# Optimization experiments

Hardware: AMD Instinct MI355X
Metric: run time of the kernel (lower is better)

## Reference

```python
import jax, jax.numpy as jnp
import numpy as np

B, T, K, H, KS = 8, 2048, 64, 8, 5
PAD = KS - 1  # causal left padding (kernel_size - stride, stride=1)


def setup_inputs() -> dict:
    key = jax.random.key(0)
    ks = jax.random.split(key, 6)
    s = 0.02
    return {
        "x": jax.random.normal(ks[0], (B, T, K), jnp.float32),
        "wq": jax.random.normal(ks[1], (K * H, K, KS), jnp.float32) * s,
        "bq": jnp.zeros((K * H,), jnp.float32),
        "wk": jax.random.normal(ks[2], (K * H, K, KS), jnp.float32) * s,
        "bk": jnp.zeros((K * H,), jnp.float32),
        "wv": jax.random.normal(ks[3], (K * H, K, KS), jnp.float32) * s,
        "wu": jax.random.normal(ks[4], (K, K * H), jnp.float32) * s,
        "bu": jnp.zeros((K,), jnp.float32),
    }


def _causal_conv(x_bkt, w, b=None):
    # x_bkt: [b, k, t]; w: [out_ch, in_ch, ks]; left-pad for causality
    y = jax.lax.conv_general_dilated(
        x_bkt, w, window_strides=(1,), padding=[(PAD, 0)],
        dimension_numbers=("NCH", "OIH", "NCH"))
    if b is not None:
        y = y + b[None, :, None]
    return y


def reference(x, wq, bq, wk, bk, wv, wu, bu):
    b, t, k = x.shape
    xc = jnp.transpose(x, (0, 2, 1))  # [b, k, t]
    # conv output channels k*h are viewed as (k, h): head index varies fastest
    q = _causal_conv(xc, wq, bq).reshape(b, k, H, t)
    kk = _causal_conv(xc, wk, bk).reshape(b, k, H, t)
    v = _causal_conv(xc, wv).reshape(b, k, H, t)
    scale = k ** 0.25
    # scores: [b, h, t_q, t_k]
    w = jnp.einsum("bdht,bdhs->bhts", q / scale, kk / scale)
    mask = jnp.triu(jnp.ones((t, t), bool), 1)  # mask_next=True, mask_diag=False
    w = jnp.where(mask[None, None], -jnp.inf, w)
    w = jax.nn.softmax(w, axis=-1)
    out = jnp.einsum("bhts,bdhs->bthd", w, v)  # [b, t, h, k]
    out = out.reshape(b, t, H * k)  # concat order (h outer, k inner)
    return out @ wu.T + bu
```

## Files before the change

kernel.cpp:

```cpp
#include <hip/hip_runtime.h>
#include <hip/hip_bf16.h>

typedef __attribute__((ext_vector_type(8))) short bf16x8;
typedef __attribute__((ext_vector_type(4))) float f32x4;
typedef __attribute__((ext_vector_type(16))) float f32x16;
typedef __attribute__((ext_vector_type(4))) unsigned int u32x4;
typedef __attribute__((ext_vector_type(2))) unsigned int u32x2;

#define Bn 8
#define Tn 2048
#define Kn 64
#define Hn 8
#define KSn 5
#define CHn 512
#define TPADn 2052

__device__ __forceinline__ unsigned short f2bf(float f) {
    unsigned int x = __builtin_bit_cast(unsigned int, f);
    unsigned int r = (x + 0x7fffu + ((x >> 16) & 1u)) >> 16;
    return (unsigned short)r;
}

__device__ __forceinline__ unsigned int cvt_pk_bf16(float lo, float hi) {
    unsigned int r;
    asm("v_cvt_pk_bf16_f32 %0, %1, %2" : "=v"(r) : "v"(lo), "v"(hi));
    return r;
}

__device__ __forceinline__ float fast_exp2(float x) {
#if __has_builtin(__builtin_amdgcn_exp2f)
    return __builtin_amdgcn_exp2f(x);
#else
    float r;
    asm("v_exp_f32 %0, %1" : "=v"(r) : "v"(x));
    return r;
#endif
}

__device__ __forceinline__ float xhalf_max(float v) {
    return fmaxf(v, __shfl_xor(v, 32));
}
__device__ __forceinline__ float xhalf_add(float v) {
    return v + __shfl_xor(v, 32);
}

__device__ __forceinline__ u32x2 pl32swap(unsigned int x, unsigned int y) {
#if __has_builtin(__builtin_amdgcn_permlane32_swap)
    return __builtin_amdgcn_permlane32_swap(x, y, false, false);
#else
    unsigned int xs = (unsigned int)__shfl_xor((int)x, 32);
    unsigned int ys = (unsigned int)__shfl_xor((int)y, 32);
    int hi = (threadIdx.x & 63) >> 5;
    u32x2 r;
    r[0] = hi ? ys : x;
    r[1] = hi ? y : xs;
    return r;
#endif
}

__device__ __forceinline__ void gload_lds16(const void* g, void* l) {
    __builtin_amdgcn_global_load_lds(
        (const __attribute__((address_space(1))) void*)g,
        (__attribute__((address_space(3))) void*)l, 16, 0, 0);
}

__global__ void prep_kernel(const float* __restrict__ x,
                            const float* __restrict__ wq, const float* __restrict__ bq,
                            const float* __restrict__ wk, const float* __restrict__ bk,
                            const float* __restrict__ wv,
                            const float* __restrict__ wu,
                            unsigned short* __restrict__ x_pad,
                            unsigned short* __restrict__ w2q, unsigned short* __restrict__ w2k,
                            unsigned short* __restrict__ w2v,
                            unsigned short* __restrict__ wu_b,
                            float* __restrict__ bqs, float* __restrict__ bks)
{
    const float inv_scale = 0.424660900144f;
    const int N0 = Bn*TPADn*Kn;
    const int N1 = KSn*CHn*Kn;
    const int total = N0 + 3*N1 + CHn*Kn + 2*CHn;
    for (int i = blockIdx.x*blockDim.x + threadIdx.x; i < total; i += gridDim.x*blockDim.x) {
        if (i < N0) {
            int b = i / (TPADn*Kn);
            int rem = i - b*(TPADn*Kn);
            int p = rem >> 6, ic = rem & 63;
            x_pad[i] = (p < 4) ? (unsigned short)0
                               : f2bf(x[((size_t)b*Tn + (p - 4))*Kn + ic]);
            continue;
        }
        int r = i - N0;
        if (r < 3*N1) {
            int conv = r / N1; int rr = r - conv*N1;
            int j = rr / (CHn*Kn); int rc = rr - j*(CHn*Kn);
            int c = rc >> 6; int ic = rc & 63;
            const float* w = (conv==0) ? wq : ((conv==1) ? wk : wv);
            float s = (conv==2) ? 1.0f : inv_scale;
            unsigned short* dst = (conv==0) ? w2q : ((conv==1) ? w2k : w2v);
            dst[rr] = f2bf(w[(c*Kn + ic)*KSn + j] * s);
            continue;
        }
        r -= 3*N1;
        if (r < CHn*Kn) { wu_b[r] = f2bf(wu[r]); continue; }
        r -= CHn*Kn;
        if (r < CHn) { bqs[r] = bq[r]*inv_scale; continue; }
        r -= CHn;
        bks[r] = bk[r]*inv_scale;
    }
}

__global__ __launch_bounds__(256) void conv_v4(
    const unsigned short* __restrict__ x_pad,
    const unsigned short* __restrict__ w2q, const unsigned short* __restrict__ w2k,
    const unsigned short* __restrict__ w2v,
    const float* __restrict__ bqs, const float* __restrict__ bks,
    unsigned short* __restrict__ q_s, unsigned short* __restrict__ k_s,
    unsigned short* __restrict__ v_t)
{
    __shared__ __align__(16) unsigned short xs[2][72*64];
    __shared__ __align__(16) unsigned short ts[64*64];
    const int tg = blockIdx.x;
    const int c0 = blockIdx.y * 64;
    const int zz = blockIdx.z;
    const int conv = zz >> 3, b = zz & 7;
    const unsigned short* w2 = (conv==0) ? w2q : ((conv==1) ? w2k : w2v);
    const float* bias = (conv==0) ? bqs : ((conv==1) ? bks : nullptr);
    unsigned short* outp = (conv==0) ? q_s : ((conv==1) ? k_s : v_t);
    const int tid = threadIdx.x;
    const int wid = tid >> 6, l = tid & 63;
    const int lr = l & 15, lh = l >> 4;
    const int wt = wid & 1, wc = wid >> 1;

    bf16x8 wf[5][2][2];
    #pragma unroll
    for (int j = 0; j < 5; ++j)
        #pragma unroll
        for (int kk = 0; kk < 2; ++kk)
            #pragma unroll
            for (int n2 = 0; n2 < 2; ++n2)
                wf[j][kk][n2] = *(const bf16x8*)
                    &w2[(j*CHn + c0 + wc*32 + n2*16 + lr)*Kn + kk*32 + lh*8];
    float bv0 = bias ? bias[c0 + wc*32 + lr]      : 0.0f;
    float bv1 = bias ? bias[c0 + wc*32 + 16 + lr] : 0.0f;

    const int swz_row = l >> 3;
    const int src_inrow = ((l & 7) << 4) ^ (swz_row << 4);

    int buf = 0;
    {
        const char* base = (const char*)(x_pad + (size_t)b*TPADn*Kn);
        int p0 = tg*512;
        for (int i = wid; i < 9; i += 4) {
            const char* src = base + (size_t)(p0 + i*8 + swz_row)*128 + src_inrow;
            gload_lds16(src, (char*)&xs[0][0] + i*1024);
        }
    }
    __syncthreads();

    for (int tt = 0; tt < 8; ++tt) {
        const int t0 = (tg*8 + tt)*64;
        if (tt < 7) {
            const char* base = (const char*)(x_pad + (size_t)b*TPADn*Kn);
            int p0 = t0 + 64;
            for (int i = wid; i < 9; i += 4) {
                const char* src = base + (size_t)(p0 + i*8 + swz_row)*128 + src_inrow;
                gload_lds16(src, (char*)&xs[buf^1][0] + i*1024);
            }
        }
        const char* xb = (const char*)&xs[buf][0];
        f32x4 acc[2][2] = {};
        #pragma unroll
        for (int j = 0; j < 5; ++j)
            #pragma unroll
            for (int kk = 0; kk < 2; ++kk) {
                #pragma unroll
                for (int m = 0; m < 2; ++m) {
                    int row = wt*32 + m*16 + lr + j;
                    bf16x8 a = *(const bf16x8*)
                        (xb + row*128 + ((kk*64 + lh*16) ^ ((row & 7) << 4)));
                    acc[m][0] = __builtin_amdgcn_mfma_f32_16x16x32_bf16(a, wf[j][kk][0], acc[m][0], 0, 0, 0);
                    acc[m][1] = __builtin_amdgcn_mfma_f32_16x16x32_bf16(a, wf[j][kk][1], acc[m][1], 0, 0, 0);
                }
            }
        __syncthreads();
        #pragma unroll
        for (int m = 0; m < 2; ++m)
            #pragma unroll
            for (int n2 = 0; n2 < 2; ++n2) {
                float bv = n2 ? bv1 : bv0;
                int cl = wc*32 + n2*16 + lr;
                #pragma unroll
                for (int reg = 0; reg < 4; ++reg) {
                    int tl = wt*32 + m*16 + lh*4 + reg;
                    ts[(tl*64 + cl) ^ ((tl & 7) << 3)] = f2bf(acc[m][n2][reg] + bv);
                }
            }
        __syncthreads();
        if (conv < 2) {
            #pragma unroll
            for (int it = 0; it < 2; ++it) {
                int idx = tid + it*256;
                int tl = idx >> 3, hl = idx & 7;
                unsigned short tmp[8];
                #pragma unroll
                for (int dl = 0; dl < 8; ++dl)
                    tmp[dl] = ts[(tl*64 + hl + 8*dl) ^ ((tl & 7) << 3)];
                size_t el = ((size_t)(b*Hn + hl)*Tn + t0 + tl)*Kn + (c0 >> 3);
                *(u32x4*)&outp[el] = *(u32x4*)tmp;
            }
        } else {
            #pragma unroll
            for (int it = 0; it < 2; ++it) {
                int idx = tid + it*256;
                int tc = idx >> 6, cl2 = idx & 63;
                int hl = cl2 & 7, dl = cl2 >> 3;
                unsigned short tmp[8];
                #pragma unroll
                for (int i2 = 0; i2 < 8; ++i2)
                    tmp[i2] = ts[((tc*8 + i2)*64 + cl2) ^ (((tc*8 + i2) & 7) << 3)];
                size_t el = ((size_t)(b*Hn + hl)*Kn + (c0 >> 3) + dl)*Tn + t0 + tc*8;
                *(u32x4*)&outp[el] = *(u32x4*)tmp;
            }
        }
        buf ^= 1;
    }
}

__global__ __launch_bounds__(256, 3) void attn_kernel(
    const unsigned short* __restrict__ q_s, const unsigned short* __restrict__ k_s,
    const unsigned short* __restrict__ v_t, unsigned short* __restrict__ attn2)
{
    __shared__ __align__(16) unsigned char lds_raw[32768];
    const int tid = threadIdx.x;
    const int wid = tid >> 6, l = tid & 63;
    const int lq = l & 31, hi = l >> 5;
    const int bx = blockIdx.x;
    const int bh = (bx & 7)*8 + ((bx >> 3) & 7);
    const int kb = bx >> 6;
    int c, t0, t1, role;
    if (kb < 24) {
        c = (wid < 2) ? (16 + kb) : (63 - kb);
        int L = c + 1, mid = L >> 1, h = wid & 1;
        t0 = h ? mid : 0; t1 = h ? L : mid;
        role = h ? 2 : 1;
    } else {
        int i = kb - 24;
        c = (wid == 0) ? i : (wid == 1) ? 7 - i : (wid == 2) ? 8 + i : 15 - i;
        t0 = 0; t1 = c + 1; role = 0;
    }
    const int qw = c * 32;
    const unsigned short* qp = q_s + (size_t)bh*Tn*Kn;
    const char* kpc = (const char*)(k_s + (size_t)bh*Tn*Kn);
    const char* vpc = (const char*)(v_t + (size_t)bh*Kn*Tn);
    unsigned short* op = attn2 + (size_t)bh*Tn*Kn;
    const int qg = qw + lq;

    char* stK = (char*)lds_raw + wid*8192;
    char* stV = stK + 4096;

    const int kSrcOff = (l >> 3)*128 + (((l & 7) ^ (l >> 3)) << 4);
    const int vSrcOff = (l >> 3)*8192 + ((l >> 2) & 1)*4096
                      + ((((l & 3) ^ ((l >> 3) & 3))) << 4);
    const char* ktp = kpc + (size_t)t0*4096 + kSrcOff;
    const char* vtp = vpc + (size_t)t0*64   + vSrcOff;
    auto stage = [&]() {
        gload_lds16(ktp,           stK);
        gload_lds16(ktp + 1024,    stK + 1024);
        gload_lds16(ktp + 2048,    stK + 2048);
        gload_lds16(ktp + 3072,    stK + 3072);
        gload_lds16(vtp,           stV);
        gload_lds16(vtp + 65536,   stV + 1024);
        gload_lds16(vtp + 131072,  stV + 2048);
        gload_lds16(vtp + 196608,  stV + 3072);
        ktp += 4096; vtp += 64;
    };

    bf16x8 qf[4];
    #pragma unroll
    for (int m = 0; m < 4; ++m)
        qf[m] = *(const bf16x8*)&qp[(qw + lq)*Kn + m*16 + hi*8];

    f32x16 o0 = (f32x16)(0.0f), o1 = (f32x16)(0.0f);
    float m_run = -1e30f, l_run = 0.f;

    const int vReadBase = (lq >> 1)*128 + (lq & 1)*64;
    const int vSwz = (lq >> 1) & 3;

    stage();
    for (int t = t0; t < t1; ++t) {
        asm volatile("s_waitcnt vmcnt(0)" ::: "memory");
        __builtin_amdgcn_sched_barrier(0);
        bf16x8 kbf[4], vbf[2][2];
        #pragma unroll
        for (int m = 0; m < 4; ++m)
            kbf[m] = *(const bf16x8*)(stK + lq*128 + ((m*32 + hi*16) ^ ((lq & 7) << 4)));
        #pragma unroll
        for (int dn = 0; dn < 2; ++dn)
            #pragma unroll
            for (int ks = 0; ks < 2; ++ks)
                vbf[dn][ks] = *(const bf16x8*)
                    (stV + dn*2048 + vReadBase + (((ks*2 + hi) ^ vSwz) << 4));
        asm volatile("s_waitcnt lgkmcnt(0)" ::: "memory");
        __builtin_amdgcn_sched_barrier(0);
        if (t + 1 < t1) stage();
        __builtin_amdgcn_sched_barrier(0);
        const int s0 = t*32;
        f32x16 s = (f32x16)(0.0f);
        #pragma unroll
        for (int m = 0; m < 4; ++m)
            s = __builtin_amdgcn_mfma_f32_32x32x16_bf16(kbf[m], qf[m], s, 0, 0, 0);
        if (t == c) {
            #pragma unroll
            for (int r = 0; r < 16; ++r) {
                int sg = s0 + (r & 3) + 8*(r >> 2) + 4*hi;
                if (sg > qg) s[r] = -1e30f;
            }
        }
        float a8[8];
        #pragma unroll
        for (int r = 0; r < 8; ++r) a8[r] = fmaxf(s[r], s[r + 8]);
        float a4_0 = fmaxf(a8[0], a8[4]), a4_1 = fmaxf(a8[1], a8[5]);
        float a4_2 = fmaxf(a8[2], a8[6]), a4_3 = fmaxf(a8[3], a8[7]);
        float mt = fmaxf(fmaxf(a4_0, a4_1), fmaxf(a4_2, a4_3));
        mt = xhalf_max(mt);
        if (!__all(mt <= m_run + 8.0f)) {
            float mn = fmaxf(m_run, mt);
            float alpha = fast_exp2(m_run - mn);
            m_run = mn;
            l_run *= alpha;
            #pragma unroll
            for (int r = 0; r < 16; ++r) { o0[r] *= alpha; o1[r] *= alpha; }
        }
        float ps[4] = {0.f, 0.f, 0.f, 0.f};
        #pragma unroll
        for (int r = 0; r < 16; ++r) {
            float p = fast_exp2(s[r] - m_run);
            s[r] = p;
            ps[r & 3] += p;
        }
        l_run += (ps[0] + ps[1]) + (ps[2] + ps[3]);
        unsigned int W[8];
        #pragma unroll
        for (int rp = 0; rp < 8; ++rp)
            W[rp] = cvt_pk_bf16(s[2*rp], s[2*rp + 1]);
        u32x4 bw[2];
        #pragma unroll
        for (int m = 0; m < 2; ++m)
            #pragma unroll
            for (int jp = 0; jp < 2; ++jp) {
                u32x2 sw = pl32swap(W[jp + 4*m], W[jp + 4*m + 2]);
                bw[m][jp]     = sw[0];
                bw[m][jp + 2] = sw[1];
            }
        o0 = __builtin_amdgcn_mfma_f32_32x32x16_bf16(vbf[0][0], __builtin_bit_cast(bf16x8, bw[0]), o0, 0, 0, 0);
        o0 = __builtin_amdgcn_mfma_f32_32x32x16_bf16(vbf[0][1], __builtin_bit_cast(bf16x8, bw[1]), o0, 0, 0, 0);
        o1 = __builtin_amdgcn_mfma_f32_32x32x16_bf16(vbf[1][0], __builtin_bit_cast(bf16x8, bw[0]), o1, 0, 0, 0);
        o1 = __builtin_amdgcn_mfma_f32_32x32x16_bf16(vbf[1][1], __builtin_bit_cast(bf16x8, bw[1]), o1, 0, 0, 0);
    }

    if (role == 2) {
        float* po = (float*)stK;
        #pragma unroll
        for (int r = 0; r < 16; ++r) {
            po[r*64 + l]        = o0[r];
            po[(16 + r)*64 + l] = o1[r];
        }
    }
    if (role) __syncthreads();
    if (role == 2) {
        float* pml = (float*)(lds_raw + (wid - 1)*8192);
        pml[l] = m_run; pml[64 + l] = l_run;
    }
    if (role) __syncthreads();
    if (role == 2) return;
    if (role == 1) {
        const float* po  = (const float*)(lds_raw + (wid + 1)*8192);
        const float* pml = (const float*)(lds_raw + wid*8192);
        float m2 = pml[l], l2 = pml[64 + l];
        float mf = fmaxf(m_run, m2);
        float a1 = fast_exp2(m_run - mf), a2 = fast_exp2(m2 - mf);
        l_run = l_run*a1 + l2*a2;
        #pragma unroll
        for (int r = 0; r < 16; ++r) {
            o0[r] = o0[r]*a1 + po[r*64 + l]*a2;
            o1[r] = o1[r]*a1 + po[(16 + r)*64 + l]*a2;
        }
    }

    float l_full = xhalf_add(l_run);
    char* myLds = stK;
    float inv_l = 1.0f / l_full;
    #pragma unroll
    for (int e = 0; e < 16; e += 2) {
        int dd = (e & 3) + 8*(e >> 2) + 4*hi;
        unsigned int wv0 = cvt_pk_bf16(o0[e]*inv_l, o0[e+1]*inv_l);
        *(unsigned int*)(myLds + ((lq*128 + dd*2)      ^ ((lq & 7) << 4))) = wv0;
        unsigned int wv1 = cvt_pk_bf16(o1[e]*inv_l, o1[e+1]*inv_l);
        *(unsigned int*)(myLds + ((lq*128 + 64 + dd*2) ^ ((lq & 7) << 4))) = wv1;
    }
    int q2 = l >> 1, hf = l & 1;
    #pragma unroll
    for (int o4 = 0; o4 < 4; ++o4) {
        u32x4 vr2 = *(u32x4*)(myLds + ((q2*128 + hf*64 + o4*16) ^ ((q2 & 7) << 4)));
        *(u32x4*)&op[(qw + q2)*Kn + hf*32 + o4*8] = vr2;
    }
}

__global__ __launch_bounds__(256) void proj_kernel(
    const unsigned short* __restrict__ attn, const unsigned short* __restrict__ wu_b,
    const float* __restrict__ bu, float* __restrict__ outp)
{
    __shared__ float red[4*16*66];
    const int r0 = blockIdx.x * 16;
    const int tid = threadIdx.x;
    const int w = tid >> 6, l = tid & 63;
    const int lr = l & 15, lh = l >> 4;
    f32x4 acc[4] = {};
    const int r = r0 + lr;
    const int bb = r >> 11, tt = r & 2047;
    #pragma unroll
    for (int ki = 0; ki < 4; ++ki) {
        int kk = w*4 + ki;
        int ch = kk*32 + lh*8;
        int hh = ch >> 6, dd = ch & 63;
        bf16x8 a = *(const bf16x8*)&attn[(size_t)((bb*Hn + hh)*Tn + tt)*Kn + dd];
        #pragma unroll
        for (int n = 0; n < 4; ++n) {
            bf16x8 bf = *(const bf16x8*)&wu_b[(n*16 + lr)*CHn + ch];
            acc[n] = __builtin_amdgcn_mfma_f32_16x16x32_bf16(a, bf, acc[n], 0, 0, 0);
        }
    }
    #pragma unroll
    for (int n = 0; n < 4; ++n)
        #pragma unroll
        for (int reg = 0; reg < 4; ++reg)
            red[w*1056 + (lh*4 + reg)*66 + n*16 + lr] = acc[n][reg];
    __syncthreads();
    #pragma unroll
    for (int it = 0; it < 4; ++it) {
        int idx = tid + it*256;
        int rl = idx >> 6, ko = idx & 63;
        float s = red[rl*66 + ko] + red[1056 + rl*66 + ko]
                + red[2112 + rl*66 + ko] + red[3168 + rl*66 + ko] + bu[ko];
        outp[(size_t)(r0 + rl)*Kn + ko] = s;
    }
}

extern "C" void kernel_launch(void* const* d_in, const int* in_sizes, int n_in,
                              void* d_out, int out_size, void* d_ws, size_t ws_size,
                              hipStream_t stream)
{
    const float* x  = (const float*)d_in[0];
    const float* wq = (const float*)d_in[1];
    const float* bq = (const float*)d_in[2];
    const float* wk = (const float*)d_in[3];
    const float* bk = (const float*)d_in[4];
    const float* wv = (const float*)d_in[5];
    const float* wu = (const float*)d_in[6];
    const float* bu = (const float*)d_in[7];
    float* outp = (float*)d_out;

    char* ws = (char*)d_ws;
    size_t off = 0;
    auto alloc = [&](size_t bytes) {
        char* p = ws + off;
        off = (off + bytes + 255) & ~(size_t)255;
        return p;
    };
    unsigned short* x_pad = (unsigned short*)alloc((size_t)Bn*TPADn*Kn*2);
    unsigned short* w2q  = (unsigned short*)alloc((size_t)KSn*CHn*Kn*2);
    unsigned short* w2k  = (unsigned short*)alloc((size_t)KSn*CHn*Kn*2);
    unsigned short* w2v  = (unsigned short*)alloc((size_t)KSn*CHn*Kn*2);
    unsigned short* wu_b = (unsigned short*)alloc((size_t)CHn*Kn*2);
    float*  bqs = (float*)alloc(CHn*4);
    float*  bks = (float*)alloc(CHn*4);
    unsigned short* q_s  = (unsigned short*)alloc((size_t)Bn*Hn*Tn*Kn*2);
    unsigned short* k_s  = (unsigned short*)alloc((size_t)Bn*Hn*Tn*Kn*2);
    unsigned short* v_t  = (unsigned short*)alloc((size_t)Bn*Hn*Tn*Kn*2);
    unsigned short* attn = (unsigned short*)alloc((size_t)Bn*Tn*CHn*2);

    prep_kernel<<<2048, 256, 0, stream>>>(x, wq, bq, wk, bk, wv, wu,
                                          x_pad, w2q, w2k, w2v, wu_b, bqs, bks);
    conv_v4<<<dim3(4, 8, 24), 256, 0, stream>>>(
        x_pad, w2q, w2k, w2v, bqs, bks, q_s, k_s, v_t);
    attn_kernel<<<1792, 256, 0, stream>>>(q_s, k_s, v_t, attn);
    proj_kernel<<<(Bn*Tn)/16, 256, 0, stream>>>(attn, wu_b, bu, outp);
}
```

Before: 126.9 us.

## Process two key tiles per attention iteration with doubled LDS staging

The attention inner loop now stages and handles two 32-wide key/value tiles per iteration. It runs both score MFMAs, then a single combined max/rescale step and the PV MFMAs for both tiles, with a single-tile tail for odd counts. This halves the per-tile waits, barriers and online-softmax rescale overhead and gives more independent MFMA work between memory waits. In exchange, LDS use doubles to 64KB and launch bounds drop from 3 to 2 blocks per CU, which lowers occupancy and adds register pressure.

```diff
diff --git a/kernel.cpp b/kernel.cpp
--- a/kernel.cpp
+++ b/kernel.cpp
@@ -225,11 +225,11 @@
     }
 }
 
-__global__ __launch_bounds__(256, 3) void attn_kernel(
+__global__ __launch_bounds__(256, 2) void attn_kernel(
     const unsigned short* __restrict__ q_s, const unsigned short* __restrict__ k_s,
     const unsigned short* __restrict__ v_t, unsigned short* __restrict__ attn2)
 {
-    __shared__ __align__(16) unsigned char lds_raw[32768];
+    __shared__ __align__(16) unsigned char lds_raw[65536];
     const int tid = threadIdx.x;
     const int wid = tid >> 6, l = tid & 63;
     const int lq = l & 31, hi = l >> 5;
@@ -254,8 +254,9 @@
     unsigned short* op = attn2 + (size_t)bh*Tn*Kn;
     const int qg = qw + lq;
 
-    char* stK = (char*)lds_raw + wid*8192;
-    char* stV = stK + 4096;
+    char* slot = (char*)lds_raw + wid*16384;
+    char* stK = slot;
+    char* stV = slot + 8192;
 
     const int kSrcOff = (l >> 3)*128 + (((l & 7) ^ (l >> 3)) << 4);
     const int vSrcOff = (l >> 3)*8192 + ((l >> 2) & 1)*4096
@@ -267,11 +268,19 @@
         gload_lds16(ktp + 1024,    stK + 1024);
         gload_lds16(ktp + 2048,    stK + 2048);
         gload_lds16(ktp + 3072,    stK + 3072);
+        gload_lds16(ktp + 4096,    stK + 4096);
+        gload_lds16(ktp + 5120,    stK + 5120);
+        gload_lds16(ktp + 6144,    stK + 6144);
+        gload_lds16(ktp + 7168,    stK + 7168);
         gload_lds16(vtp,           stV);
         gload_lds16(vtp + 65536,   stV + 1024);
         gload_lds16(vtp + 131072,  stV + 2048);
         gload_lds16(vtp + 196608,  stV + 3072);
-        ktp += 4096; vtp += 64;
+        gload_lds16(vtp + 64,           stV + 4096);
+        gload_lds16(vtp + 64 + 65536,   stV + 5120);
+        gload_lds16(vtp + 64 + 131072,  stV + 6144);
+        gload_lds16(vtp + 64 + 196608,  stV + 7168);
+        ktp += 8192; vtp += 128;
     };
 
     bf16x8 qf[4];
@@ -282,17 +291,110 @@
     f32x16 o0 = (f32x16)(0.0f), o1 = (f32x16)(0.0f);
     float m_run = -1e30f, l_run = 0.f;
 
+    const int kReadBase = lq*128;
+    const int kReadSwz  = (lq & 7) << 4;
     const int vReadBase = (lq >> 1)*128 + (lq & 1)*64;
     const int vSwz = (lq >> 1) & 3;
 
     stage();
-    for (int t = t0; t < t1; ++t) {
+    int t = t0;
+    while (t + 1 < t1) {
+        asm volatile("s_waitcnt vmcnt(0)" ::: "memory");
+        __builtin_amdgcn_sched_barrier(0);
+        bf16x8 k0[4], k1[4], v0[2][2], v1[2][2];
+        #pragma unroll
+        for (int m = 0; m < 4; ++m) {
+            k0[m] = *(const bf16x8*)(stK +        kReadBase + ((m*32 + hi*16) ^ kReadSwz));
+            k1[m] = *(const bf16x8*)(stK + 4096 + kReadBase + ((m*32 + hi*16) ^ kReadSwz));
+        }
+        #pragma unroll
+        for (int dn = 0; dn < 2; ++dn)
+            #pragma unroll
+            for (int ks = 0; ks < 2; ++ks) {
+                v0[dn][ks] = *(const bf16x8*)
+                    (stV +        dn*2048 + vReadBase + (((ks*2 + hi) ^ vSwz) << 4));
+                v1[dn][ks] = *(const bf16x8*)
+                    (stV + 4096 + dn*2048 + vReadBase + (((ks*2 + hi) ^ vSwz) << 4));
+            }
+        asm volatile("s_waitcnt lgkmcnt(0)" ::: "memory");
+        __builtin_amdgcn_sched_barrier(0);
+        if (t + 2 < t1) stage();
+        __builtin_amdgcn_sched_barrier(0);
+        f32x16 s = (f32x16)(0.0f), s2 = (f32x16)(0.0f);
+        #pragma unroll
+        for (int m = 0; m < 4; ++m)
+            s  = __builtin_amdgcn_mfma_f32_32x32x16_bf16(k0[m], qf[m], s, 0, 0, 0);
+        #pragma unroll
+        for (int m = 0; m < 4; ++m)
+            s2 = __builtin_amdgcn_mfma_f32_32x32x16_bf16(k1[m], qf[m], s2, 0, 0, 0);
+        if (t + 1 == c) {
+            const int s0g = (t + 1)*32;
+            #pragma unroll
+            for (int r = 0; r < 16; ++r) {
+                int sg = s0g + (r & 3) + 8*(r >> 2) + 4*hi;
+                if (sg > qg) s2[r] = -1e30f;
+            }
+        }
+        float a8[8];
+        #pragma unroll
+        for (int r = 0; r < 8; ++r)
+            a8[r] = fmaxf(fmaxf(s[r], s[r + 8]), fmaxf(s2[r], s2[r + 8]));
+        float a4_0 = fmaxf(a8[0], a8[4]), a4_1 = fmaxf(a8[1], a8[5]);
+        float a4_2 = fmaxf(a8[2], a8[6]), a4_3 = fmaxf(a8[3], a8[7]);
+        float mt = fmaxf(fmaxf(a4_0, a4_1), fmaxf(a4_2, a4_3));
+        mt = xhalf_max(mt);
+        if (!__all(mt <= m_run + 8.0f)) {
+            float mn = fmaxf(m_run, mt);
+            float alpha = fast_exp2(m_run - mn);
+            m_run = mn;
+            l_run *= alpha;
+            #pragma unroll
+            for (int r = 0; r < 16; ++r) { o0[r] *= alpha; o1[r] *= alpha; }
+        }
+        float ps[4] = {0.f, 0.f, 0.f, 0.f};
+        #pragma unroll
+        for (int r = 0; r < 16; ++r) {
+            float p = fast_exp2(s[r] - m_run);
+            s[r] = p; ps[r & 3] += p;
+            float p2 = fast_exp2(s2[r] - m_run);
+            s2[r] = p2; ps[r & 3] += p2;
+        }
+        l_run += (ps[0] + ps[1]) + (ps[2] + ps[3]);
+        unsigned int W[8], W2[8];
+        #pragma unroll
+        for (int rp = 0; rp < 8; ++rp) {
+            W[rp]  = cvt_pk_bf16(s[2*rp],  s[2*rp + 1]);
+            W2[rp] = cvt_pk_bf16(s2[2*rp], s2[2*rp + 1]);
+        }
+        u32x4 bw[2], bw2[2];
+        #pragma unroll
+        for (int m = 0; m < 2; ++m)
+            #pragma unroll
+            for (int jp = 0; jp < 2; ++jp) {
+                u32x2 sw = pl32swap(W[jp + 4*m], W[jp + 4*m + 2]);
+                bw[m][jp]     = sw[0];
+                bw[m][jp + 2] = sw[1];
+                u32x2 sw2 = pl32swap(W2[jp + 4*m], W2[jp + 4*m + 2]);
+                bw2[m][jp]     = sw2[0];
+                bw2[m][jp + 2] = sw2[1];
+            }
+        o0 = __builtin_amdgcn_mfma_f32_32x32x16_bf16(v0[0][0], __builtin_bit_cast(bf16x8, bw[0]),  o0, 0, 0, 0);
+        o0 = __builtin_amdgcn_mfma_f32_32x32x16_bf16(v0[0][1], __builtin_bit_cast(bf16x8, bw[1]),  o0, 0, 0, 0);
+        o0 = __builtin_amdgcn_mfma_f32_32x32x16_bf16(v1[0][0], __builtin_bit_cast(bf16x8, bw2[0]), o0, 0, 0, 0);
+        o0 = __builtin_amdgcn_mfma_f32_32x32x16_bf16(v1[0][1], __builtin_bit_cast(bf16x8, bw2[1]), o0, 0, 0, 0);
+        o1 = __builtin_amdgcn_mfma_f32_32x32x16_bf16(v0[1][0], __builtin_bit_cast(bf16x8, bw[0]),  o1, 0, 0, 0);
+        o1 = __builtin_amdgcn_mfma_f32_32x32x16_bf16(v0[1][1], __builtin_bit_cast(bf16x8, bw[1]),  o1, 0, 0, 0);
+        o1 = __builtin_amdgcn_mfma_f32_32x32x16_bf16(v1[1][0], __builtin_bit_cast(bf16x8, bw2[0]), o1, 0, 0, 0);
+        o1 = __builtin_amdgcn_mfma_f32_32x32x16_bf16(v1[1][1], __builtin_bit_cast(bf16x8, bw2[1]), o1, 0, 0, 0);
+        t += 2;
+    }
+    if (t < t1) {
         asm volatile("s_waitcnt vmcnt(0)" ::: "memory");
         __builtin_amdgcn_sched_barrier(0);
         bf16x8 kbf[4], vbf[2][2];
         #pragma unroll
         for (int m = 0; m < 4; ++m)
-            kbf[m] = *(const bf16x8*)(stK + lq*128 + ((m*32 + hi*16) ^ ((lq & 7) << 4)));
+            kbf[m] = *(const bf16x8*)(stK + kReadBase + ((m*32 + hi*16) ^ kReadSwz));
         #pragma unroll
         for (int dn = 0; dn < 2; ++dn)
             #pragma unroll
@@ -300,8 +402,6 @@
                 vbf[dn][ks] = *(const bf16x8*)
                     (stV + dn*2048 + vReadBase + (((ks*2 + hi) ^ vSwz) << 4));
         asm volatile("s_waitcnt lgkmcnt(0)" ::: "memory");
-        __builtin_amdgcn_sched_barrier(0);
-        if (t + 1 < t1) stage();
         __builtin_amdgcn_sched_barrier(0);
         const int s0 = t*32;
         f32x16 s = (f32x16)(0.0f);
@@ -358,7 +458,7 @@
     }
 
     if (role == 2) {
-        float* po = (float*)stK;
+        float* po = (float*)slot;
         #pragma unroll
         for (int r = 0; r < 16; ++r) {
             po[r*64 + l]        = o0[r];
@@ -367,14 +467,14 @@
     }
     if (role) __syncthreads();
     if (role == 2) {
-        float* pml = (float*)(lds_raw + (wid - 1)*8192);
+        float* pml = (float*)(lds_raw + (wid - 1)*16384 + 8704);
         pml[l] = m_run; pml[64 + l] = l_run;
     }
     if (role) __syncthreads();
     if (role == 2) return;
     if (role == 1) {
-        const float* po  = (const float*)(lds_raw + (wid + 1)*8192);
-        const float* pml = (const float*)(lds_raw + wid*8192);
+        const float* po  = (const float*)(lds_raw + (wid + 1)*16384);
+        const float* pml = (const float*)(lds_raw + wid*16384 + 8704);
         float m2 = pml[l], l2 = pml[64 + l];
         float mf = fmaxf(m_run, m2);
         float a1 = fast_exp2(m_run - mf), a2 = fast_exp2(m2 - mf);
@@ -387,7 +487,7 @@
     }
 
     float l_full = xhalf_add(l_run);
-    char* myLds = stK;
+    char* myLds = slot;
     float inv_l = 1.0f / l_full;
     #pragma unroll
     for (int e = 0; e < 16; e += 2) {
```

Result: slower. 129.9 us (+2.4%).

## Share K/V tiles across four consecutive query waves in attention block

Applied to the files above, without the earlier changes.

Each block now handles four consecutive 32-row query chunks of one head. All four waves cooperatively stage each K/V tile into a shared double-buffered LDS tile synchronized with __syncthreads, replacing per-wave private staging with a split-KV merge. This cuts redundant global K/V loads and LDS use, which allows higher occupancy (launch bounds 4) and fewer blocks. The cost is load imbalance inside a block, since lower waves idle while the block runs to the last wave's causal limit, plus a block barrier every step.

```diff
diff --git a/kernel.cpp b/kernel.cpp
--- a/kernel.cpp
+++ b/kernel.cpp
@@ -225,53 +225,35 @@
     }
 }
 
-__global__ __launch_bounds__(256, 3) void attn_kernel(
+__global__ __launch_bounds__(256, 4) void attn_kernel(
     const unsigned short* __restrict__ q_s, const unsigned short* __restrict__ k_s,
     const unsigned short* __restrict__ v_t, unsigned short* __restrict__ attn2)
 {
-    __shared__ __align__(16) unsigned char lds_raw[32768];
+    __shared__ __align__(16) unsigned char lds_raw[16384];
     const int tid = threadIdx.x;
     const int wid = tid >> 6, l = tid & 63;
     const int lq = l & 31, hi = l >> 5;
     const int bx = blockIdx.x;
     const int bh = (bx & 7)*8 + ((bx >> 3) & 7);
-    const int kb = bx >> 6;
-    int c, t0, t1, role;
-    if (kb < 24) {
-        c = (wid < 2) ? (16 + kb) : (63 - kb);
-        int L = c + 1, mid = L >> 1, h = wid & 1;
-        t0 = h ? mid : 0; t1 = h ? L : mid;
-        role = h ? 2 : 1;
-    } else {
-        int i = kb - 24;
-        c = (wid == 0) ? i : (wid == 1) ? 7 - i : (wid == 2) ? 8 + i : 15 - i;
-        t0 = 0; t1 = c + 1; role = 0;
-    }
-    const int qw = c * 32;
+    const int s4g = (bx >> 6) & 3, g = bx >> 8;
+    const int j = (g == 0) ? s4g : (g == 1) ? 15 - s4g : (g == 2) ? 7 - s4g : 8 + s4g;
+    const int cmax = 4*j + 3;
+    const int cw = 4*j + wid;
+    const int qw = cw * 32;
     const unsigned short* qp = q_s + (size_t)bh*Tn*Kn;
     const char* kpc = (const char*)(k_s + (size_t)bh*Tn*Kn);
     const char* vpc = (const char*)(v_t + (size_t)bh*Kn*Tn);
     unsigned short* op = attn2 + (size_t)bh*Tn*Kn;
     const int qg = qw + lq;
 
-    char* stK = (char*)lds_raw + wid*8192;
-    char* stV = stK + 4096;
-
-    const int kSrcOff = (l >> 3)*128 + (((l & 7) ^ (l >> 3)) << 4);
-    const int vSrcOff = (l >> 3)*8192 + ((l >> 2) & 1)*4096
-                      + ((((l & 3) ^ ((l >> 3) & 3))) << 4);
-    const char* ktp = kpc + (size_t)t0*4096 + kSrcOff;
-    const char* vtp = vpc + (size_t)t0*64   + vSrcOff;
-    auto stage = [&]() {
-        gload_lds16(ktp,           stK);
-        gload_lds16(ktp + 1024,    stK + 1024);
-        gload_lds16(ktp + 2048,    stK + 2048);
-        gload_lds16(ktp + 3072,    stK + 3072);
-        gload_lds16(vtp,           stV);
-        gload_lds16(vtp + 65536,   stV + 1024);
-        gload_lds16(vtp + 131072,  stV + 2048);
-        gload_lds16(vtp + 196608,  stV + 3072);
-        ktp += 4096; vtp += 64;
+    const int krow = wid*8 + (l >> 3);
+    const char* kSrc0 = kpc + krow*128 + (((l & 7) ^ (krow & 7)) << 4);
+    const char* vSrc0 = vpc + (size_t)krow*8192 + ((l >> 2) & 1)*4096
+                      + ((((l & 3) ^ (krow & 3))) << 4);
+    const int dstOff = wid*1024;
+    auto stage = [&](int pp, int t) {
+        gload_lds16(kSrc0 + (size_t)t*4096, lds_raw + pp*4096 + dstOff);
+        gload_lds16(vSrc0 + (size_t)t*64,   lds_raw + 8192 + pp*4096 + dstOff);
     };
 
     bf16x8 qf[4];
@@ -282,112 +264,88 @@
     f32x16 o0 = (f32x16)(0.0f), o1 = (f32x16)(0.0f);
     float m_run = -1e30f, l_run = 0.f;
 
+    const int kReadBase = lq*128;
+    const int kReadSwz  = (lq & 7) << 4;
     const int vReadBase = (lq >> 1)*128 + (lq & 1)*64;
     const int vSwz = (lq >> 1) & 3;
 
-    stage();
-    for (int t = t0; t < t1; ++t) {
-        asm volatile("s_waitcnt vmcnt(0)" ::: "memory");
-        __builtin_amdgcn_sched_barrier(0);
-        bf16x8 kbf[4], vbf[2][2];
-        #pragma unroll
-        for (int m = 0; m < 4; ++m)
-            kbf[m] = *(const bf16x8*)(stK + lq*128 + ((m*32 + hi*16) ^ ((lq & 7) << 4)));
-        #pragma unroll
-        for (int dn = 0; dn < 2; ++dn)
-            #pragma unroll
-            for (int ks = 0; ks < 2; ++ks)
-                vbf[dn][ks] = *(const bf16x8*)
-                    (stV + dn*2048 + vReadBase + (((ks*2 + hi) ^ vSwz) << 4));
-        asm volatile("s_waitcnt lgkmcnt(0)" ::: "memory");
-        __builtin_amdgcn_sched_barrier(0);
-        if (t + 1 < t1) stage();
-        __builtin_amdgcn_sched_barrier(0);
-        const int s0 = t*32;
-        f32x16 s = (f32x16)(0.0f);
-        #pragma unroll
-        for (int m = 0; m < 4; ++m)
-            s = __builtin_amdgcn_mfma_f32_32x32x16_bf16(kbf[m], qf[m], s, 0, 0, 0);
-        if (t == c) {
+    stage(0, 0);
+    __syncthreads();
+    int p = 0;
+    for (int t = 0; t <= cmax; ++t) {
+        if (t < cmax) stage(p ^ 1, t + 1);
+        if (t <= cw) {
+            const char* sK = (const char*)lds_raw + p*4096;
+            const char* sV = (const char*)lds_raw + 8192 + p*4096;
+            bf16x8 kbf[4], vbf[2][2];
+            #pragma unroll
+            for (int m = 0; m < 4; ++m)
+                kbf[m] = *(const bf16x8*)(sK + kReadBase + ((m*32 + hi*16) ^ kReadSwz));
+            #pragma unroll
+            for (int dn = 0; dn < 2; ++dn)
+                #pragma unroll
+                for (int ks = 0; ks < 2; ++ks)
+                    vbf[dn][ks] = *(const bf16x8*)
+                        (sV + dn*2048 + vReadBase + (((ks*2 + hi) ^ vSwz) << 4));
+            const int s0 = t*32;
+            f32x16 s = (f32x16)(0.0f);
+            #pragma unroll
+            for (int m = 0; m < 4; ++m)
+                s = __builtin_amdgcn_mfma_f32_32x32x16_bf16(kbf[m], qf[m], s, 0, 0, 0);
+            if (t == cw) {
+                #pragma unroll
+                for (int r = 0; r < 16; ++r) {
+                    int sg = s0 + (r & 3) + 8*(r >> 2) + 4*hi;
+                    if (sg > qg) s[r] = -1e30f;
+                }
+            }
+            float a8[8];
+            #pragma unroll
+            for (int r = 0; r < 8; ++r) a8[r] = fmaxf(s[r], s[r + 8]);
+            float a4_0 = fmaxf(a8[0], a8[4]), a4_1 = fmaxf(a8[1], a8[5]);
+            float a4_2 = fmaxf(a8[2], a8[6]), a4_3 = fmaxf(a8[3], a8[7]);
+            float mt = fmaxf(fmaxf(a4_0, a4_1), fmaxf(a4_2, a4_3));
+            mt = xhalf_max(mt);
+            if (!__all(mt <= m_run + 8.0f)) {
+                float mn = fmaxf(m_run, mt);
+                float alpha = fast_exp2(m_run - mn);
+                m_run = mn;
+                l_run *= alpha;
+                #pragma unroll
+                for (int r = 0; r < 16; ++r) { o0[r] *= alpha; o1[r] *= alpha; }
+            }
+            float ps[4] = {0.f, 0.f, 0.f, 0.f};
             #pragma unroll
             for (int r = 0; r < 16; ++r) {
-                int sg = s0 + (r & 3) + 8*(r >> 2) + 4*hi;
-                if (sg > qg) s[r] = -1e30f;
-            }
-        }
-        float a8[8];
-        #pragma unroll
-        for (int r = 0; r < 8; ++r) a8[r] = fmaxf(s[r], s[r + 8]);
-        float a4_0 = fmaxf(a8[0], a8[4]), a4_1 = fmaxf(a8[1], a8[5]);
-        float a4_2 = fmaxf(a8[2], a8[6]), a4_3 = fmaxf(a8[3], a8[7]);
-        float mt = fmaxf(fmaxf(a4_0, a4_1), fmaxf(a4_2, a4_3));
-        mt = xhalf_max(mt);
-        if (!__all(mt <= m_run + 8.0f)) {
-            float mn = fmaxf(m_run, mt);
-            float alpha = fast_exp2(m_run - mn);
-            m_run = mn;
-            l_run *= alpha;
-            #pragma unroll
-            for (int r = 0; r < 16; ++r) { o0[r] *= alpha; o1[r] *= alpha; }
-        }
-        float ps[4] = {0.f, 0.f, 0.f, 0.f};
-        #pragma unroll
-        for (int r = 0; r < 16; ++r) {
-            float p = fast_exp2(s[r] - m_run);
-            s[r] = p;
-            ps[r & 3] += p;
-        }
-        l_run += (ps[0] + ps[1]) + (ps[2] + ps[3]);
-        unsigned int W[8];
-        #pragma unroll
-        for (int rp = 0; rp < 8; ++rp)
-            W[rp] = cvt_pk_bf16(s[2*rp], s[2*rp + 1]);
-        u32x4 bw[2];
-        #pragma unroll
-        for (int m = 0; m < 2; ++m)
-            #pragma unroll
-            for (int jp = 0; jp < 2; ++jp) {
-                u32x2 sw = pl32swap(W[jp + 4*m], W[jp + 4*m + 2]);
-                bw[m][jp]     = sw[0];
-                bw[m][jp + 2] = sw[1];
-            }
-        o0 = __builtin_amdgcn_mfma_f32_32x32x16_bf16(vbf[0][0], __builtin_bit_cast(bf16x8, bw[0]), o0, 0, 0, 0);
-        o0 = __builtin_amdgcn_mfma_f32_32x32x16_bf16(vbf[0][1], __builtin_bit_cast(bf16x8, bw[1]), o0, 0, 0, 0);
-        o1 = __builtin_amdgcn_mfma_f32_32x32x16_bf16(vbf[1][0], __builtin_bit_cast(bf16x8, bw[0]), o1, 0, 0, 0);
-        o1 = __builtin_amdgcn_mfma_f32_32x32x16_bf16(vbf[1][1], __builtin_bit_cast(bf16x8, bw[1]), o1, 0, 0, 0);
-    }
-
-    if (role == 2) {
-        float* po = (float*)stK;
-        #pragma unroll
-        for (int r = 0; r < 16; ++r) {
-            po[r*64 + l]        = o0[r];
-            po[(16 + r)*64 + l] = o1[r];
-        }
-    }
-    if (role) __syncthreads();
-    if (role == 2) {
-        float* pml = (float*)(lds_raw + (wid - 1)*8192);
-        pml[l] = m_run; pml[64 + l] = l_run;
-    }
-    if (role) __syncthreads();
-    if (role == 2) return;
-    if (role == 1) {
-        const float* po  = (const float*)(lds_raw + (wid + 1)*8192);
-        const float* pml = (const float*)(lds_raw + wid*8192);
-        float m2 = pml[l], l2 = pml[64 + l];
-        float mf = fmaxf(m_run, m2);
-        float a1 = fast_exp2(m_run - mf), a2 = fast_exp2(m2 - mf);
-        l_run = l_run*a1 + l2*a2;
-        #pragma unroll
-        for (int r = 0; r < 16; ++r) {
-            o0[r] = o0[r]*a1 + po[r*64 + l]*a2;
-            o1[r] = o1[r]*a1 + po[(16 + r)*64 + l]*a2;
-        }
+                float pv = fast_exp2(s[r] - m_run);
+                s[r] = pv;
+                ps[r & 3] += pv;
+            }
+            l_run += (ps[0] + ps[1]) + (ps[2] + ps[3]);
+            unsigned int W[8];
+            #pragma unroll
+            for (int rp = 0; rp < 8; ++rp)
+                W[rp] = cvt_pk_bf16(s[2*rp], s[2*rp + 1]);
+            u32x4 bw[2];
+            #pragma unroll
+            for (int m = 0; m < 2; ++m)
+                #pragma unroll
+                for (int jp = 0; jp < 2; ++jp) {
+                    u32x2 sw = pl32swap(W[jp + 4*m], W[jp + 4*m + 2]);
+                    bw[m][jp]     = sw[0];
+                    bw[m][jp + 2] = sw[1];
+                }
+            o0 = __builtin_amdgcn_mfma_f32_32x32x16_bf16(vbf[0][0], __builtin_bit_cast(bf16x8, bw[0]), o0, 0, 0, 0);
+            o0 = __builtin_amdgcn_mfma_f32_32x32x16_bf16(vbf[0][1], __builtin_bit_cast(bf16x8, bw[1]), o0, 0, 0, 0);
+            o1 = __builtin_amdgcn_mfma_f32_32x32x16_bf16(vbf[1][0], __builtin_bit_cast(bf16x8, bw[0]), o1, 0, 0, 0);
+            o1 = __builtin_amdgcn_mfma_f32_32x32x16_bf16(vbf[1][1], __builtin_bit_cast(bf16x8, bw[1]), o1, 0, 0, 0);
+        }
+        __syncthreads();
+        p ^= 1;
     }
 
     float l_full = xhalf_add(l_run);
-    char* myLds = stK;
+    char* myLds = (char*)lds_raw + wid*4096;
     float inv_l = 1.0f / l_full;
     #pragma unroll
     for (int e = 0; e < 16; e += 2) {
@@ -482,6 +440,6 @@
                                           x_pad, w2q, w2k, w2v, wu_b, bqs, bks);
     conv_v4<<<dim3(4, 8, 24), 256, 0, stream>>>(
         x_pad, w2q, w2k, w2v, bqs, bks, q_s, k_s, v_t);
-    attn_kernel<<<1792, 256, 0, stream>>>(q_s, k_s, v_t, attn);
+    attn_kernel<<<1024, 256, 0, stream>>>(q_s, k_s, v_t, attn);
     proj_kernel<<<(Bn*Tn)/16, 256, 0, stream>>>(attn, wu_b, bu, outp);
 }
```

Measured after the change: 114.8 us. 9.5% less time.
